# Performance work log

Measured on AMD Instinct MI355X. Metric: run time of the kernel, lower is better.

## Reference

```python
import jax, jax.numpy as jnp
import numpy as np

N_NODES = 100000
N_FEAT = 128
HIDDEN = 64
OUT = 16
N_EDGES = 3200000
N_POS = 500000
N_NEG = 500000


def setup_inputs() -> dict:
    key = jax.random.key(0)
    ks = jax.random.split(key, 8)
    x = jax.random.normal(ks[0], (N_NODES, N_FEAT), dtype=jnp.float32)
    edge_index = jax.random.randint(ks[1], (2, N_EDGES), 0, N_NODES, dtype=jnp.int64)
    pos_edge_index = jax.random.randint(ks[2], (2, N_POS), 0, N_NODES, dtype=jnp.int64)
    neg_edge_index = jax.random.randint(ks[3], (2, N_NEG), 0, N_NODES, dtype=jnp.int64)
    W1 = jax.random.normal(ks[4], (N_FEAT, HIDDEN), dtype=jnp.float32) * (1.0 / np.sqrt(N_FEAT))
    b1 = jnp.zeros((HIDDEN,), dtype=jnp.float32)
    W2 = jax.random.normal(ks[5], (HIDDEN, OUT), dtype=jnp.float32) * (1.0 / np.sqrt(HIDDEN))
    b2 = jnp.zeros((OUT,), dtype=jnp.float32)
    return {"x": x, "edge_index": edge_index, "pos_edge_index": pos_edge_index,
            "neg_edge_index": neg_edge_index, "W1": W1, "b1": b1, "W2": W2, "b2": b2}


def gcn_conv(x, W, b, src, dst):
    """PyG GCNConv with add_self_loops=True: D^-1/2 (A+I) D^-1/2 X W + b."""
    n = x.shape[0]
    h = x @ W  # [N, out]
    # degree including self-loop (+1)
    deg = jax.ops.segment_sum(jnp.ones(dst.shape, dtype=h.dtype), dst, num_segments=n) + 1.0
    dis = jax.lax.rsqrt(deg)  # deg >= 1, never inf
    coef = dis[src] * dis[dst]  # [E]
    agg = jax.ops.segment_sum(h[src] * coef[:, None], dst, num_segments=n)
    # self-loop message: norm = dis[i]*dis[i]
    agg = agg + h * (dis * dis)[:, None]
    return agg + b


def reference(x, edge_index, pos_edge_index, neg_edge_index, W1, b1, W2, b2):
    src, dst = edge_index[0], edge_index[1]
    z = jax.nn.relu(gcn_conv(x, W1, b1, src, dst))
    z = gcn_conv(z, W2, b2, src, dst)  # [N, 16]
    ei = jnp.concatenate([pos_edge_index, neg_edge_index], axis=-1)  # [2, P+Q]
    logits = jnp.sum(z[ei[0]] * z[ei[1]], axis=-1)  # [P+Q]
    return logits
```

## Files before the change

### kernel.cpp

```cpp
#include <hip/hip_runtime.h>

#define F 128
#define H 64
#define O 16

#define BSHIFT 7
#define BSZ 128
#define NSUB 16
#define SUBCAP 384
#define ACHUNK 8192
#define XS 136

typedef _Float16 half8_t __attribute__((ext_vector_type(8)));
typedef _Float16 half4_t __attribute__((ext_vector_type(4)));
typedef float f32x4 __attribute__((ext_vector_type(4)));

__global__ void k_prep(const float* __restrict__ W1, _Float16* __restrict__ wt_hi,
                       _Float16* __restrict__ wt_lo, int* __restrict__ bcur, int NC) {
    int i = blockIdx.x * blockDim.x + threadIdx.x;
    if (i < NC) bcur[i] = i * SUBCAP;
    if (i < H * F) {
        int c = i >> 7, k = i & 127;
        float w = W1[k * H + c];
        _Float16 hi = (_Float16)w;
        wt_hi[i] = hi;
        wt_lo[i] = (_Float16)(w - (float)hi);
    }
}

__global__ __launch_bounds__(512) void k_bucketA(const int* __restrict__ src,
                                                 const int* __restrict__ dstv,
                                                 int* __restrict__ bcur,
                                                 int* __restrict__ bdata, int E) {
    __shared__ int hist[1024];
    for (int t = threadIdx.x; t < 1024; t += 512) hist[t] = 0;
    __syncthreads();
    int base = blockIdx.x * ACHUNK;
    int end = min(base + ACHUNK, E);
    int tid = threadIdx.x;
    for (int i = base + tid * 4; i + 3 < end; i += 2048) {
        int4 d4 = *(const int4*)(dstv + i);
        atomicAdd(&hist[d4.x >> BSHIFT], 1);
        atomicAdd(&hist[d4.y >> BSHIFT], 1);
        atomicAdd(&hist[d4.z >> BSHIFT], 1);
        atomicAdd(&hist[d4.w >> BSHIFT], 1);
    }
    for (int i = base + ((end - base) & ~3) + tid; i < end; i += 512)
        atomicAdd(&hist[dstv[i] >> BSHIFT], 1);
    __syncthreads();
    int sub = blockIdx.x & (NSUB - 1);
    for (int b = tid; b < 1024; b += 512) {
        int c = hist[b];
        if (c > 0) hist[b] = atomicAdd(&bcur[b * NSUB + sub], c);
    }
    __syncthreads();
    for (int i = base + tid * 4; i + 3 < end; i += 2048) {
        int4 s4 = *(const int4*)(src + i);
        int4 d4 = *(const int4*)(dstv + i);
        int p0 = atomicAdd(&hist[d4.x >> BSHIFT], 1);
        bdata[p0] = (s4.x << BSHIFT) | (d4.x & (BSZ - 1));
        int p1 = atomicAdd(&hist[d4.y >> BSHIFT], 1);
        bdata[p1] = (s4.y << BSHIFT) | (d4.y & (BSZ - 1));
        int p2 = atomicAdd(&hist[d4.z >> BSHIFT], 1);
        bdata[p2] = (s4.z << BSHIFT) | (d4.z & (BSZ - 1));
        int p3 = atomicAdd(&hist[d4.w >> BSHIFT], 1);
        bdata[p3] = (s4.w << BSHIFT) | (d4.w & (BSZ - 1));
    }
    for (int i = base + ((end - base) & ~3) + tid; i < end; i += 512) {
        int d = dstv[i];
        int pos = atomicAdd(&hist[d >> BSHIFT], 1);
        bdata[pos] = (src[i] << BSHIFT) | (d & (BSZ - 1));
    }
}

__global__ void k_bscan(const int* __restrict__ bcur, int* __restrict__ bstart, int NBK) {
    __shared__ int s[1024];
    int tid = threadIdx.x;
    int tot = 0;
    if (tid < NBK) {
        for (int ss = 0; ss < NSUB; ss++)
            tot += bcur[tid * NSUB + ss] - (tid * NSUB + ss) * SUBCAP;
    }
    s[tid] = tot;
    __syncthreads();
    for (int off = 1; off < 1024; off <<= 1) {
        int v = (tid >= off) ? s[tid - off] : 0;
        __syncthreads();
        s[tid] += v;
        __syncthreads();
    }
    bstart[tid] = s[tid] - tot;
}

__global__ __launch_bounds__(256) void k_bplace(const int* __restrict__ bdata,
                                                const int* __restrict__ bcur,
                                                const int* __restrict__ bstart,
                                                int* __restrict__ row_ptr,
                                                float* __restrict__ dis,
                                                int* __restrict__ col, int N) {
    __shared__ int h[BSZ];
    __shared__ int pref[BSZ];
    __shared__ int cur[BSZ];
    int b = blockIdx.x;
    int node0 = b << BSHIFT;
    int nloc = min(BSZ, N - node0);
    int tid = threadIdx.x;
    if (tid < BSZ) h[tid] = 0;
    __syncthreads();
    for (int s = 0; s < NSUB; s++) {
        int start = (b * NSUB + s) * SUBCAP;
        int end = bcur[b * NSUB + s];
        for (int p = start + tid; p < end; p += 256)
            atomicAdd(&h[bdata[p] & (BSZ - 1)], 1);
    }
    __syncthreads();
    int myDeg = 0;
    if (tid < BSZ) {
        myDeg = h[tid];
        pref[tid] = myDeg;
    }
    __syncthreads();
    for (int off = 1; off < BSZ; off <<= 1) {
        int v = (tid < BSZ && tid >= off) ? pref[tid - off] : 0;
        __syncthreads();
        if (tid < BSZ) pref[tid] += v;
        __syncthreads();
    }
    int base = bstart[b];
    if (tid < nloc) {
        int excl = base + pref[tid] - myDeg;
        cur[tid] = excl;
        row_ptr[node0 + tid] = excl;
        dis[node0 + tid] = rsqrtf((float)myDeg + 1.0f);
    }
    if (tid == 0) row_ptr[node0 + nloc] = base + pref[BSZ - 1];
    __syncthreads();
    for (int s = 0; s < NSUB; s++) {
        int start = (b * NSUB + s) * SUBCAP;
        int end = bcur[b * NSUB + s];
        for (int p = start + tid; p < end; p += 256) {
            int v = bdata[p];
            int pos = atomicAdd(&cur[v & (BSZ - 1)], 1);
            col[pos] = v >> BSHIFT;
        }
    }
}

__global__ __launch_bounds__(256) void k_gemm1(const float* __restrict__ x,
                                               const _Float16* __restrict__ wt_hi,
                                               const _Float16* __restrict__ wt_lo,
                                               const float* __restrict__ dis,
                                               _Float16* __restrict__ h1p, int N) {
    __shared__ _Float16 xh[64 * XS], xl[64 * XS], wh[64 * XS], wl[64 * XS];
    int tid = threadIdx.x;
    int row0 = blockIdx.x * 64;
#pragma unroll
    for (int i = 0; i < 8; i++) {
        int idx = i * 256 + tid;
        int r = idx >> 5;
        int c = (idx & 31) * 4;
        int rr = row0 + r; if (rr >= N) rr = N - 1;
        float4 v = *(const float4*)(x + (size_t)rr * F + c);
        half4_t h = {(_Float16)v.x, (_Float16)v.y, (_Float16)v.z, (_Float16)v.w};
        half4_t l = {(_Float16)(v.x - (float)h[0]), (_Float16)(v.y - (float)h[1]),
                     (_Float16)(v.z - (float)h[2]), (_Float16)(v.w - (float)h[3])};
        *(half4_t*)(xh + r * XS + c) = h;
        *(half4_t*)(xl + r * XS + c) = l;
    }
#pragma unroll
    for (int i = 0; i < 4; i++) {
        int idx = i * 256 + tid;
        int c = idx >> 4;
        int k8 = (idx & 15) * 8;
        *(half8_t*)(wh + c * XS + k8) = *(const half8_t*)(wt_hi + c * 128 + k8);
        *(half8_t*)(wl + c * XS + k8) = *(const half8_t*)(wt_lo + c * 128 + k8);
    }
    __syncthreads();
    int wv = tid >> 6, lane = tid & 63;
    int m = lane & 15, qd = lane >> 4;
    const _Float16* xhp = xh + (wv * 16 + m) * XS;
    const _Float16* xlp = xl + (wv * 16 + m) * XS;
    f32x4 acc[4] = {f32x4{0,0,0,0}, f32x4{0,0,0,0}, f32x4{0,0,0,0}, f32x4{0,0,0,0}};
#pragma unroll
    for (int kc = 0; kc < 4; kc++) {
        int ko = kc * 32 + qd * 8;
        half8_t ah = *(const half8_t*)(xhp + ko);
        half8_t al = *(const half8_t*)(xlp + ko);
#pragma unroll
        for (int nt = 0; nt < 4; nt++) {
            half8_t bh = *(const half8_t*)(wh + (nt * 16 + m) * XS + ko);
            half8_t bl = *(const half8_t*)(wl + (nt * 16 + m) * XS + ko);
            acc[nt] = __builtin_amdgcn_mfma_f32_16x16x32_f16(ah, bh, acc[nt], 0, 0, 0);
            acc[nt] = __builtin_amdgcn_mfma_f32_16x16x32_f16(ah, bl, acc[nt], 0, 0, 0);
            acc[nt] = __builtin_amdgcn_mfma_f32_16x16x32_f16(al, bh, acc[nt], 0, 0, 0);
        }
    }
#pragma unroll
    for (int reg = 0; reg < 4; reg++) {
        int row = row0 + wv * 16 + qd * 4 + reg;
        if (row < N) {
            float d = dis[row];
#pragma unroll
            for (int nt = 0; nt < 4; nt++) {
                h1p[(size_t)row * H + nt * 16 + m] = (_Float16)(acc[nt][reg] * d);
            }
        }
    }
}

__global__ __launch_bounds__(256) void k_gather1(const _Float16* __restrict__ h1p,
                                                 const float* __restrict__ dis,
                                                 const int* __restrict__ row_ptr,
                                                 const int* __restrict__ col,
                                                 const float* __restrict__ b1,
                                                 const float* __restrict__ W2,
                                                 _Float16* __restrict__ h2p, int N) {
    __shared__ float w2t[16 * 65];
    int tid = threadIdx.x;
    {
        int idx = tid * 4;
        float4 v = *(const float4*)(W2 + idx);
        const float* vp = (const float*)&v;
#pragma unroll
        for (int i = 0; i < 4; i++) {
            int e = idx + i;
            w2t[(e & 15) * 65 + (e >> 4)] = vp[i];
        }
    }
    __syncthreads();
    int node = blockIdx.x * 4 + (tid >> 6);
    int lane = tid & 63;
    int g = lane >> 3;
    int t = lane & 7;
    if (node < N) {
        const half8_t* hp = (const half8_t*)h1p;
        float acc[8];
#pragma unroll
        for (int j = 0; j < 8; j++) acc[j] = 0.f;
        int e = row_ptr[node + 1];
        int p = row_ptr[node] + g;
        for (; p + 8 < e; p += 16) {
            int s0 = col[p], s1 = col[p + 8];
            half8_t v0 = hp[(size_t)s0 * 8 + t];
            half8_t v1 = hp[(size_t)s1 * 8 + t];
#pragma unroll
            for (int j = 0; j < 8; j++) acc[j] += (float)v0[j];
#pragma unroll
            for (int j = 0; j < 8; j++) acc[j] += (float)v1[j];
        }
        if (p < e) {
            int s0 = col[p];
            half8_t v0 = hp[(size_t)s0 * 8 + t];
#pragma unroll
            for (int j = 0; j < 8; j++) acc[j] += (float)v0[j];
        }
#pragma unroll
        for (int off = 8; off < 64; off <<= 1) {
#pragma unroll
            for (int j = 0; j < 8; j++) acc[j] += __shfl_xor(acc[j], off);
        }
        float dn = dis[node];
        half8_t self = hp[(size_t)node * 8 + t];
        float o[8];
#pragma unroll
        for (int j = 0; j < 8; j++)
            o[j] = fmaxf(fmaf(acc[j] + (float)self[j], dn, b1[t * 8 + j]), 0.f);
        const float* w1r = w2t + g * 65 + t * 8;
        const float* w2r = w2t + (g + 8) * 65 + t * 8;
        float p1 = 0.f, p2 = 0.f;
#pragma unroll
        for (int j = 0; j < 8; j++) {
            p1 = fmaf(o[j], w1r[j], p1);
            p2 = fmaf(o[j], w2r[j], p2);
        }
#pragma unroll
        for (int off = 1; off < 8; off <<= 1) {
            p1 += __shfl_xor(p1, off);
            p2 += __shfl_xor(p2, off);
        }
        if (t == 0) {
            h2p[(size_t)node * O + g]     = (_Float16)(p1 * dn);
            h2p[(size_t)node * O + g + 8] = (_Float16)(p2 * dn);
        }
    }
}

__global__ __launch_bounds__(256) void k_gather2(const _Float16* __restrict__ h2p,
                                                 const float* __restrict__ dis,
                                                 const int* __restrict__ row_ptr,
                                                 const int* __restrict__ col,
                                                 const float* __restrict__ b2,
                                                 float* __restrict__ z2, int N) {
    int node = blockIdx.x * 4 + (threadIdx.x >> 6);
    if (node >= N) return;
    int lane = threadIdx.x & 63;
    int g = lane >> 1;
    int t = lane & 1;
    const half8_t* hp = (const half8_t*)h2p;
    float acc[8];
#pragma unroll
    for (int j = 0; j < 8; j++) acc[j] = 0.f;
    int e = row_ptr[node + 1];
    for (int p = row_ptr[node] + g; p < e; p += 32) {
        int s = col[p];
        half8_t v = hp[(size_t)s * 2 + t];
#pragma unroll
        for (int j = 0; j < 8; j++) acc[j] += (float)v[j];
    }
#pragma unroll
    for (int off = 2; off < 64; off <<= 1) {
#pragma unroll
        for (int j = 0; j < 8; j++) acc[j] += __shfl_xor(acc[j], off);
    }
    if (g == 0) {
        float dn = dis[node];
        half8_t self = hp[(size_t)node * 2 + t];
        float o[8];
#pragma unroll
        for (int j = 0; j < 8; j++)
            o[j] = fmaf(acc[j] + (float)self[j], dn, b2[t * 8 + j]);
        float4* zp = (float4*)(z2 + (size_t)node * O + t * 8);
        zp[0] = float4{o[0], o[1], o[2], o[3]};
        zp[1] = float4{o[4], o[5], o[6], o[7]};
    }
}

__global__ __launch_bounds__(256) void k_logits(const float* __restrict__ z2,
                                                const int* __restrict__ pos,
                                                const int* __restrict__ neg,
                                                float* __restrict__ out, int P, int Q) {
    int tid = blockIdx.x * 256 + threadIdx.x;
    int i = tid >> 2;
    if (i >= P + Q) return;
    int k = tid & 3;
    int a, b;
    if (i < P) { a = pos[i]; b = pos[P + i]; }
    else       { int t = i - P; a = neg[t]; b = neg[Q + t]; }
    float4 va = *(const float4*)(z2 + (size_t)a * O + k * 4);
    float4 vb = *(const float4*)(z2 + (size_t)b * O + k * 4);
    float r = va.x * vb.x + va.y * vb.y + va.z * vb.z + va.w * vb.w;
    r += __shfl_xor(r, 1);
    r += __shfl_xor(r, 2);
    if (k == 0) out[i] = r;
}

extern "C" void kernel_launch(void* const* d_in, const int* in_sizes, int n_in,
                              void* d_out, int out_size, void* d_ws, size_t ws_size,
                              hipStream_t stream) {
    const float* x   = (const float*)d_in[0];
    const int*   ei  = (const int*)d_in[1];
    const int*   pos = (const int*)d_in[2];
    const int*   neg = (const int*)d_in[3];
    const float* W1  = (const float*)d_in[4];
    const float* b1  = (const float*)d_in[5];
    const float* W2  = (const float*)d_in[6];
    const float* b2  = (const float*)d_in[7];
    float* out = (float*)d_out;

    int N = in_sizes[0] / F;
    int E = in_sizes[1] / 2;
    int P = in_sizes[2] / 2;
    int Q = in_sizes[3] / 2;
    const int* src  = ei;
    const int* dstv = ei + E;

    int Npad = ((N + 255) / 256) * 256;
    int Epad = (E + 63) & ~63;
    int NBK = (N + BSZ - 1) / BSZ;
    int NC  = NBK * NSUB;

    char* w = (char*)d_ws;
    float*    dis     = (float*)w;    w += (size_t)Npad * 4;
    int*      row_ptr = (int*)w;      w += (size_t)(Npad + 256) * 4;
    int*      bcur    = (int*)w;      w += 16384 * 4;
    int*      bstart  = (int*)w;      w += 1024 * 4;
    int*      col     = (int*)w;      w += (size_t)Epad * 4;
    _Float16* h1p     = (_Float16*)w;
    int*      bdata   = (int*)w;
    size_t h1b = (size_t)N * H * 2, bdb = (size_t)NC * SUBCAP * 4;
    w += (h1b > bdb ? h1b : bdb);
    _Float16* h2p     = (_Float16*)w; w += (size_t)N * O * 2;
    float*    z2      = (float*)w;    w += (size_t)N * O * 4;
    _Float16* wt_hi   = (_Float16*)w; w += (size_t)H * F * 2;
    _Float16* wt_lo   = (_Float16*)w;

    int prepN = (NC > H * F) ? NC : H * F;

    k_prep<<<(prepN + 255) / 256, 256, 0, stream>>>(W1, wt_hi, wt_lo, bcur, NC);
    k_bucketA<<<(E + ACHUNK - 1) / ACHUNK, 512, 0, stream>>>(src, dstv, bcur, bdata, E);
    k_bscan<<<1, 1024, 0, stream>>>(bcur, bstart, NBK);
    k_bplace<<<NBK, 256, 0, stream>>>(bdata, bcur, bstart, row_ptr, dis, col, N);

    k_gemm1<<<(N + 63) / 64, 256, 0, stream>>>(x, wt_hi, wt_lo, dis, h1p, N);
    k_gather1<<<(N + 3) / 4, 256, 0, stream>>>(h1p, dis, row_ptr, col, b1, W2, h2p, N);
    k_gather2<<<(N + 3) / 4, 256, 0, stream>>>(h2p, dis, row_ptr, col, b2, z2, N);
    k_logits<<<((P + Q) * 4 + 255) / 256, 256, 0, stream>>>(z2, pos, neg, out, P, Q);
}
```

Before: 330.7 us.

## Use persistent grid-stride gathers with fused fp16 mix-accumulate and deeper unroll

Both gather kernels now launch a fixed grid of 2048 blocks and stride over nodes. This amortizes the W2 transpose into shared memory, the bias loads and the block launch cost. The inner accumulation uses inline v_fma_mix_f32 asm to add fp16 values straight into fp32 accumulators without separate converts. gather1 also unrolls to four outstanding row loads per iteration for more memory-level parallelism. The self-loop term is folded into the accumulator by lane group 0, which removes a separate load per lane. The inline asm ties the code to gfx ISA op_sel semantics, and a fixed grid may underfill the GPU or cause tail imbalance.

```diff
diff --git a/kernel.cpp b/kernel.cpp
--- a/kernel.cpp
+++ b/kernel.cpp
@@ -14,6 +14,22 @@
 typedef _Float16 half8_t __attribute__((ext_vector_type(8)));
 typedef _Float16 half4_t __attribute__((ext_vector_type(4)));
 typedef float f32x4 __attribute__((ext_vector_type(4)));
+
+#define MIX2(alo, ahi, dw)                                                              \
+    do {                                                                                \
+        asm("v_fma_mix_f32 %0, %1, 1.0, %0 op_sel_hi:[1,0,0]"                           \
+            : "+v"(alo) : "v"(dw));                                                     \
+        asm("v_fma_mix_f32 %0, %1, 1.0, %0 op_sel:[1,0,0] op_sel_hi:[1,0,0]"            \
+            : "+v"(ahi) : "v"(dw));                                                     \
+    } while (0)
+
+#define MIXROW(r)                                                                       \
+    do {                                                                                \
+        MIX2(acc[0], acc[1], (r).x);                                                    \
+        MIX2(acc[2], acc[3], (r).y);                                                    \
+        MIX2(acc[4], acc[5], (r).z);                                                    \
+        MIX2(acc[6], acc[7], (r).w);                                                    \
+    } while (0)
 
 __global__ void k_prep(const float* __restrict__ W1, _Float16* __restrict__ wt_hi,
                        _Float16* __restrict__ wt_lo, int* __restrict__ bcur, int NC) {
@@ -228,31 +244,44 @@
         }
     }
     __syncthreads();
-    int node = blockIdx.x * 4 + (tid >> 6);
     int lane = tid & 63;
     int g = lane >> 3;
     int t = lane & 7;
-    if (node < N) {
-        const half8_t* hp = (const half8_t*)h1p;
+    const int4* hp4 = (const int4*)h1p;
+    float bb[8];
+#pragma unroll
+    for (int j = 0; j < 8; j++) bb[j] = b1[t * 8 + j];
+    const float* w1r = w2t + g * 65 + t * 8;
+    const float* w2r = w2t + (g + 8) * 65 + t * 8;
+
+    for (int node = blockIdx.x * 4 + (tid >> 6); node < N; node += gridDim.x * 4) {
         float acc[8];
 #pragma unroll
         for (int j = 0; j < 8; j++) acc[j] = 0.f;
         int e = row_ptr[node + 1];
         int p = row_ptr[node] + g;
+        for (; p + 24 < e; p += 32) {
+            int s0 = col[p], s1 = col[p + 8], s2 = col[p + 16], s3 = col[p + 24];
+            int4 r0 = hp4[(size_t)s0 * 8 + t];
+            int4 r1 = hp4[(size_t)s1 * 8 + t];
+            int4 r2 = hp4[(size_t)s2 * 8 + t];
+            int4 r3 = hp4[(size_t)s3 * 8 + t];
+            MIXROW(r0); MIXROW(r1); MIXROW(r2); MIXROW(r3);
+        }
         for (; p + 8 < e; p += 16) {
             int s0 = col[p], s1 = col[p + 8];
-            half8_t v0 = hp[(size_t)s0 * 8 + t];
-            half8_t v1 = hp[(size_t)s1 * 8 + t];
-#pragma unroll
-            for (int j = 0; j < 8; j++) acc[j] += (float)v0[j];
-#pragma unroll
-            for (int j = 0; j < 8; j++) acc[j] += (float)v1[j];
+            int4 r0 = hp4[(size_t)s0 * 8 + t];
+            int4 r1 = hp4[(size_t)s1 * 8 + t];
+            MIXROW(r0); MIXROW(r1);
         }
         if (p < e) {
             int s0 = col[p];
-            half8_t v0 = hp[(size_t)s0 * 8 + t];
-#pragma unroll
-            for (int j = 0; j < 8; j++) acc[j] += (float)v0[j];
+            int4 r0 = hp4[(size_t)s0 * 8 + t];
+            MIXROW(r0);
+        }
+        if (g == 0) {
+            int4 rs = hp4[(size_t)node * 8 + t];
+            MIXROW(rs);
         }
 #pragma unroll
         for (int off = 8; off < 64; off <<= 1) {
@@ -260,13 +289,10 @@
             for (int j = 0; j < 8; j++) acc[j] += __shfl_xor(acc[j], off);
         }
         float dn = dis[node];
-        half8_t self = hp[(size_t)node * 8 + t];
         float o[8];
 #pragma unroll
         for (int j = 0; j < 8; j++)
-            o[j] = fmaxf(fmaf(acc[j] + (float)self[j], dn, b1[t * 8 + j]), 0.f);
-        const float* w1r = w2t + g * 65 + t * 8;
-        const float* w2r = w2t + (g + 8) * 65 + t * 8;
+            o[j] = fmaxf(fmaf(acc[j], dn, bb[j]), 0.f);
         float p1 = 0.f, p2 = 0.f;
 #pragma unroll
         for (int j = 0; j < 8; j++) {
@@ -291,37 +317,44 @@
                                                  const int* __restrict__ col,
                                                  const float* __restrict__ b2,
                                                  float* __restrict__ z2, int N) {
-    int node = blockIdx.x * 4 + (threadIdx.x >> 6);
-    if (node >= N) return;
-    int lane = threadIdx.x & 63;
+    int tid = threadIdx.x;
+    int lane = tid & 63;
     int g = lane >> 1;
     int t = lane & 1;
-    const half8_t* hp = (const half8_t*)h2p;
-    float acc[8];
-#pragma unroll
-    for (int j = 0; j < 8; j++) acc[j] = 0.f;
-    int e = row_ptr[node + 1];
-    for (int p = row_ptr[node] + g; p < e; p += 32) {
-        int s = col[p];
-        half8_t v = hp[(size_t)s * 2 + t];
-#pragma unroll
-        for (int j = 0; j < 8; j++) acc[j] += (float)v[j];
-    }
-#pragma unroll
-    for (int off = 2; off < 64; off <<= 1) {
-#pragma unroll
-        for (int j = 0; j < 8; j++) acc[j] += __shfl_xor(acc[j], off);
-    }
-    if (g == 0) {
-        float dn = dis[node];
-        half8_t self = hp[(size_t)node * 2 + t];
-        float o[8];
-#pragma unroll
-        for (int j = 0; j < 8; j++)
-            o[j] = fmaf(acc[j] + (float)self[j], dn, b2[t * 8 + j]);
-        float4* zp = (float4*)(z2 + (size_t)node * O + t * 8);
-        zp[0] = float4{o[0], o[1], o[2], o[3]};
-        zp[1] = float4{o[4], o[5], o[6], o[7]};
+    const int4* hp4 = (const int4*)h2p;
+    float bb[8];
+#pragma unroll
+    for (int j = 0; j < 8; j++) bb[j] = b2[t * 8 + j];
+
+    for (int node = blockIdx.x * 4 + (tid >> 6); node < N; node += gridDim.x * 4) {
+        float acc[8];
+#pragma unroll
+        for (int j = 0; j < 8; j++) acc[j] = 0.f;
+        int e = row_ptr[node + 1];
+        for (int p = row_ptr[node] + g; p < e; p += 32) {
+            int s = col[p];
+            int4 r = hp4[(size_t)s * 2 + t];
+            MIXROW(r);
+        }
+        if (g == 0) {
+            int4 rs = hp4[(size_t)node * 2 + t];
+            MIXROW(rs);
+        }
+#pragma unroll
+        for (int off = 2; off < 64; off <<= 1) {
+#pragma unroll
+            for (int j = 0; j < 8; j++) acc[j] += __shfl_xor(acc[j], off);
+        }
+        if (g == 0) {
+            float dn = dis[node];
+            float o[8];
+#pragma unroll
+            for (int j = 0; j < 8; j++)
+                o[j] = fmaf(acc[j], dn, bb[j]);
+            float4* zp = (float4*)(z2 + (size_t)node * O + t * 8);
+            zp[0] = float4{o[0], o[1], o[2], o[3]};
+            zp[1] = float4{o[4], o[5], o[6], o[7]};
+        }
     }
 }
 
@@ -392,7 +425,7 @@
     k_bplace<<<NBK, 256, 0, stream>>>(bdata, bcur, bstart, row_ptr, dis, col, N);
 
     k_gemm1<<<(N + 63) / 64, 256, 0, stream>>>(x, wt_hi, wt_lo, dis, h1p, N);
-    k_gather1<<<(N + 3) / 4, 256, 0, stream>>>(h1p, dis, row_ptr, col, b1, W2, h2p, N);
-    k_gather2<<<(N + 3) / 4, 256, 0, stream>>>(h2p, dis, row_ptr, col, b2, z2, N);
+    k_gather1<<<2048, 256, 0, stream>>>(h1p, dis, row_ptr, col, b1, W2, h2p, N);
+    k_gather2<<<2048, 256, 0, stream>>>(h2p, dis, row_ptr, col, b2, z2, N);
     k_logits<<<((P + Q) * 4 + 255) / 256, 256, 0, stream>>>(z2, pos, neg, out, P, Q);
 }
```

After: 328.2 us. No clear change (-0.7%).
